# Optimization experiments

Hardware: AMD Instinct MI355X
Metric: run time of the kernel (lower is better)

## Reference

```python
import jax, jax.numpy as jnp
import numpy as np

B, T, C, H = 4, 2048, 1024, 16
D = C // H
SCALE = float(np.sqrt(C / H))  # quadf_scale = sqrt(D) = 8.0


def setup_inputs() -> dict:
    key = jax.random.key(0)
    k1, k2, k3 = jax.random.split(key, 3)
    x = jax.random.normal(k1, (B, T, C), dtype=jnp.float32)
    # torch Linear(C, 3C): y = x @ W.T; we store the transposed weight [C, 3C]
    W_attn = jax.random.normal(k2, (C, 3 * C), dtype=jnp.float32) * 0.02
    W_proj = jax.random.normal(k3, (C, C), dtype=jnp.float32) * 0.02
    return {"x": x, "W_attn": W_attn, "W_proj": W_proj}


def reference(x, W_attn, W_proj):
    # QKV projection
    qkv = x @ W_attn                      # [B, T, 3C]
    q, k, v = jnp.split(qkv, 3, axis=-1)  # each [B, T, C]

    def heads(t):  # [B, T, C] -> [B, H, T, D]
        return t.reshape(B, T, H, D).transpose(0, 2, 1, 3)

    q, k, v = heads(q), heads(k), heads(v)

    # scaled dot-product scores with causal mask
    scores = jnp.einsum("bhtd,bhsd->bhts", q, k) / SCALE  # [B, H, T, T]
    causal = jnp.tril(jnp.ones((T, T), dtype=bool))
    scores = jnp.where(causal, scores, -jnp.inf)
    attn = jax.nn.softmax(scores, axis=-1)
    # dropout = 0.0 (eval mode), so omitted

    y = jnp.einsum("bhts,bhsd->bhtd", attn, v)            # [B, H, T, D]
    y = y.transpose(0, 2, 1, 3).reshape(B, T, C)
    return y @ W_proj
```

## Files before the change

### kernel.cpp

```cpp
#include <hip/hip_runtime.h>
#include <hip/hip_bf16.h>

#define B_ 4
#define T_ 2048
#define C_ 1024
#define H_ 16
#define D_ 64
#define C3 3072

typedef __bf16 bf16x8 __attribute__((ext_vector_type(8)));
typedef __bf16 bf16x4 __attribute__((ext_vector_type(4)));
typedef float f32x2 __attribute__((ext_vector_type(2)));
typedef float f32x4 __attribute__((ext_vector_type(4)));
typedef float f32x16 __attribute__((ext_vector_type(16)));
typedef unsigned u32x4 __attribute__((ext_vector_type(4)));

#define SCALE_LOG2E 0.1803368801111244f

__device__ __forceinline__ void gload_lds16(const void* g, void* lds) {
  __builtin_amdgcn_global_load_lds((const __attribute__((address_space(1))) void*)g,
                                   (__attribute__((address_space(3))) void*)lds, 16, 0, 0);
}

__device__ __forceinline__ int swz128(int row, int chunk) {
  return row * 128 + ((chunk ^ (row & 7)) << 4);
}

__device__ __forceinline__ unsigned cvt_pk_bf16(float a, float b) {
  unsigned r;
  asm("v_cvt_pk_bf16_f32 %0, %1, %2" : "=v"(r) : "v"(a), "v"(b));
  return r;
}

__device__ __forceinline__ void pl32swap(unsigned& x, unsigned& y) {
  asm volatile("v_permlane32_swap_b32 %0, %1" : "+v"(x), "+v"(y));
}

__device__ __forceinline__ float fmax3(float a, float b, float c) {
  float d;
  asm("v_max3_f32 %0, %1, %2, %3" : "=v"(d) : "v"(a), "v"(b), "v"(c));
  return d;
}

__device__ __forceinline__ f32x2 pk_add(f32x2 a, f32x2 b) {
  f32x2 d;
  asm("v_pk_add_f32 %0, %1, %2" : "=v"(d) : "v"(a), "v"(b));
  return d;
}

__global__ void cast_x_kernel(const float* __restrict__ in, __bf16* __restrict__ out, int n4) {
  int i = blockIdx.x * blockDim.x + threadIdx.x;
  if (i >= n4) return;
  float4 v = ((const float4*)in)[i];
  bf16x4 o;
  o.x = (__bf16)v.x; o.y = (__bf16)v.y; o.z = (__bf16)v.z; o.w = (__bf16)v.w;
  ((bf16x4*)out)[i] = o;
}

__global__ void transpose_cast_kernel(const float* __restrict__ in, __bf16* __restrict__ out,
                                      int K, int N) {
  __shared__ float tile[32][33];
  int kb = blockIdx.y * 32, nb = blockIdx.x * 32;
  int tx = threadIdx.x, ty = threadIdx.y;
#pragma unroll
  for (int i = 0; i < 4; i++) {
    int r = ty + i * 8;
    tile[r][tx] = in[(size_t)(kb + r) * N + nb + tx];
  }
  __syncthreads();
#pragma unroll
  for (int i = 0; i < 4; i++) {
    int r = ty + i * 8;
    out[(size_t)(nb + r) * K + kb + tx] = (__bf16)tile[tx][r];
  }
}

template <int MODE>
__global__ __launch_bounds__(256) void gemm_bt_kernel(const __bf16* __restrict__ A,
                                                      const __bf16* __restrict__ Bt,
                                                      __bf16* __restrict__ Cb,
                                                      float* __restrict__ Cf,
                                                      __bf16* __restrict__ vT,
                                                      int M, int N, int K) {
  __shared__ char ldsbuf[2 * 128 * 128];
  char* ldsA = ldsbuf;
  char* ldsB = ldsbuf + 128 * 128;
  int tid = threadIdx.x, w = tid >> 6, l = tid & 63;
  int gx = gridDim.x;
  int nwg = gx * gridDim.y;
  int orig = blockIdx.y * gx + blockIdx.x;
  int cpx = nwg >> 3;
  int swz = (orig & 7) * cpx + (orig >> 3);
  int bx = swz % gx, by = swz / gx;
  int m0 = by * 128, n0 = bx * 128;
  int wr = w >> 1, wc = w & 1;
  int lr = l & 15, lhi = l >> 4;
  f32x4 acc[4][4];
#pragma unroll
  for (int m = 0; m < 4; m++)
#pragma unroll
    for (int n = 0; n < 4; n++) acc[m][n] = (f32x4){0.f, 0.f, 0.f, 0.f};

  int nK = K >> 6;
  for (int kt = 0; kt < nK; kt++) {
    int k0 = kt << 6;
    __syncthreads();
#pragma unroll
    for (int jj = 0; jj < 4; jj++) {
      int q = w * 4 + jj;
      int row = q * 8 + (l >> 3);
      int cg = (l & 7) ^ ((l >> 3) & 7);
      gload_lds16(A + (size_t)(m0 + row) * K + k0 + cg * 8, ldsA + q * 1024);
      gload_lds16(Bt + (size_t)(n0 + row) * K + k0 + cg * 8, ldsB + q * 1024);
    }
    __syncthreads();
    bf16x8 af[4][2], bfr[4][2];
#pragma unroll
    for (int m = 0; m < 4; m++) {
      int r = wr * 64 + m * 16 + lr;
#pragma unroll
      for (int kc = 0; kc < 2; kc++)
        af[m][kc] = *(const bf16x8*)(ldsA + swz128(r, kc * 4 + lhi));
    }
#pragma unroll
    for (int n = 0; n < 4; n++) {
      int r = wc * 64 + n * 16 + lr;
#pragma unroll
      for (int kc = 0; kc < 2; kc++)
        bfr[n][kc] = *(const bf16x8*)(ldsB + swz128(r, kc * 4 + lhi));
    }
#pragma unroll
    for (int kc = 0; kc < 2; kc++)
#pragma unroll
      for (int m = 0; m < 4; m++)
#pragma unroll
        for (int n = 0; n < 4; n++)
          acc[m][n] =
              __builtin_amdgcn_mfma_f32_16x16x32_bf16(af[m][kc], bfr[n][kc], acc[m][n], 0, 0, 0);
  }

  if (MODE == 2 && n0 >= 2048) {
    int bb = m0 >> 11;
    int tb = (m0 & 2047) + wr * 64 + lhi * 4;
#pragma unroll
    for (int n = 0; n < 4; n++) {
      int vcol = (n0 - 2048) + wc * 64 + n * 16 + lr;
      __bf16* vp = vT + ((size_t)bb * 1024 + vcol) * T_;
#pragma unroll
      for (int m = 0; m < 4; m++) {
        bf16x4 pv;
#pragma unroll
        for (int i = 0; i < 4; i++) pv[i] = (__bf16)acc[m][n][i];
        *(bf16x4*)(vp + tb + m * 16) = pv;
      }
    }
    return;
  }

  float oscale = (MODE == 2 && n0 < 1024) ? SCALE_LOG2E : 1.0f;
#pragma unroll
  for (int m = 0; m < 4; m++)
#pragma unroll
    for (int n = 0; n < 4; n++)
#pragma unroll
      for (int i = 0; i < 4; i++) {
        int rg = m0 + wr * 64 + m * 16 + lhi * 4 + i;
        int cg = n0 + wc * 64 + n * 16 + lr;
        if (MODE == 1)
          Cf[(size_t)rg * N + cg] = acc[m][n][i];
        else
          Cb[(size_t)rg * N + cg] = (__bf16)(acc[m][n][i] * oscale);
      }
}

__global__ __launch_bounds__(256) void attn_kernel(const __bf16* __restrict__ qkv,
                                                   const __bf16* __restrict__ vT,
                                                   __bf16* __restrict__ y) {
  __shared__ __align__(16) char lds[2][16384];
  int tid = threadIdx.x, w = tid >> 6, l = tid & 63;

  int g = blockIdx.x >> 6, bh = blockIdx.x & 63;
  int q2 = g >> 2;
  int qb = (q2 & 1) ? ((q2 == 1) ? g + 4 : g - 12) : (15 - g);
  int b = bh >> 4, h = bh & 15;
  size_t base = (size_t)b * T_ * C3;
  int lq = l & 31, hi = l >> 5;
  int qrow = qb * 128 + w * 32 + lq;
  int q0w = qb * 128 + w * 32;

  int lrow = l >> 3;
  int cg = (l & 7) ^ (lrow & 7);
  const __bf16* kptr = qkv + base + (size_t)(w * 16 + lrow) * C3 + C_ + h * D_ + cg * 8;
  const __bf16* vptr = vT + ((size_t)bh * D_ + w * 16 + lrow) * T_ + cg * 8;

  bf16x8 qf[4];
  {
    const __bf16* qp = qkv + base + (size_t)qrow * C3 + h * D_;
#pragma unroll
    for (int c = 0; c < 4; c++) qf[c] = *(const bf16x8*)(qp + c * 16 + hi * 8);
  }

  f32x16 zacc;
#pragma unroll
  for (int i = 0; i < 16; i++) zacc[i] = 0.f;
  f32x16 o[2];
  o[0] = zacc; o[1] = zacc;
  float mrun = -__builtin_inff(), lrun = 0.f;

  int nt = 2 * qb + 2;

  {
    char* kb = &lds[0][0];
    char* vb = &lds[0][8192];
    gload_lds16(kptr, kb + w * 2048);
    gload_lds16(kptr + 8 * C3, kb + w * 2048 + 1024);
    gload_lds16(vptr, vb + w * 2048);
    gload_lds16(vptr + 8 * T_, vb + w * 2048 + 1024);
  }

  for (int kt = 0; kt < nt; kt++) {
    int buf = kt & 1;
    __syncthreads();
    if (kt + 1 < nt) {
      char* kb = &lds[buf ^ 1][0];
      char* vb = &lds[buf ^ 1][8192];
      const __bf16* kp = kptr + (size_t)(kt + 1) * 64 * C3;
      const __bf16* vp = vptr + (kt + 1) * 64;
      gload_lds16(kp, kb + w * 2048);
      gload_lds16(kp + 8 * C3, kb + w * 2048 + 1024);
      gload_lds16(vp, vb + w * 2048);
      gload_lds16(vp + 8 * T_, vb + w * 2048 + 1024);
    }
    if (kt * 64 > q0w + 31) continue;
    char* kb = &lds[buf][0];
    char* vb = &lds[buf][8192];

    f32x16 s[2];
    __builtin_amdgcn_s_setprio(1);
#pragma unroll
    for (int b2 = 0; b2 < 2; b2++) {
      bf16x8 kf0 = *(const bf16x8*)(kb + swz128(b2 * 32 + lq, hi));
      s[b2] = __builtin_amdgcn_mfma_f32_32x32x16_bf16(kf0, qf[0], zacc, 0, 0, 0);
#pragma unroll
      for (int c = 1; c < 4; c++) {
        bf16x8 kf = *(const bf16x8*)(kb + swz128(b2 * 32 + lq, 2 * c + hi));
        s[b2] = __builtin_amdgcn_mfma_f32_32x32x16_bf16(kf, qf[c], s[b2], 0, 0, 0);
      }
    }
    __builtin_amdgcn_s_setprio(0);

    if (kt * 64 + 63 > q0w) {
#pragma unroll
      for (int b2 = 0; b2 < 2; b2++)
#pragma unroll
        for (int r = 0; r < 16; r++) {
          int kv = kt * 64 + b2 * 32 + ((r & 3) + 8 * (r >> 2)) + 4 * hi;
          if (kv > qrow) s[b2][r] = -1e30f;
        }
    }

    {
      auto xi = [&](int i) -> float { return i < 16 ? s[0][i] : s[1][i - 16]; };
      float t10[11];
#pragma unroll
      for (int g3 = 0; g3 < 10; g3++) t10[g3] = fmax3(xi(3 * g3), xi(3 * g3 + 1), xi(3 * g3 + 2));
      t10[10] = fmaxf(xi(30), xi(31));
      float u0 = fmax3(t10[0], t10[1], t10[2]);
      float u1 = fmax3(t10[3], t10[4], t10[5]);
      float u2 = fmax3(t10[6], t10[7], t10[8]);
      float u3 = fmaxf(t10[9], t10[10]);
      float tl = fmaxf(fmax3(u0, u1, u2), u3);
      float tmax = fmaxf(tl, __shfl_xor(tl, 32));

      if (!__all(tmax - mrun <= 8.0f)) {
        float mnew = fmaxf(mrun, tmax);
        float al = __builtin_amdgcn_exp2f(mrun - mnew);
        mrun = mnew;
        lrun *= al;
#pragma unroll
        for (int d = 0; d < 2; d++)
#pragma unroll
          for (int i = 0; i < 16; i++) o[d][i] *= al;
      }
    }

#pragma unroll
    for (int b2 = 0; b2 < 2; b2++)
#pragma unroll
      for (int r = 0; r < 16; r++) s[b2][r] = __builtin_amdgcn_exp2f(s[b2][r] - mrun);

    {
      f32x2 p8[8];
#pragma unroll
      for (int g3 = 0; g3 < 8; g3++) {
        f32x2 a = {s[0][2 * g3], s[0][2 * g3 + 1]};
        f32x2 b2v = {s[1][2 * g3], s[1][2 * g3 + 1]};
        p8[g3] = pk_add(a, b2v);
      }
#pragma unroll
      for (int g3 = 0; g3 < 4; g3++) p8[g3] = pk_add(p8[g3], p8[g3 + 4]);
      p8[0] = pk_add(p8[0], p8[2]);
      p8[1] = pk_add(p8[1], p8[3]);
      p8[0] = pk_add(p8[0], p8[1]);
      float rs = p8[0][0] + p8[0][1];
      lrun += rs + __shfl_xor(rs, 32);
    }

    bf16x8 pa[4];
#pragma unroll
    for (int b2 = 0; b2 < 2; b2++) {
      unsigned wg[4][2];
#pragma unroll
      for (int gg = 0; gg < 4; gg++) {
        wg[gg][0] = cvt_pk_bf16(s[b2][4 * gg + 0], s[b2][4 * gg + 1]);
        wg[gg][1] = cvt_pk_bf16(s[b2][4 * gg + 2], s[b2][4 * gg + 3]);
      }
#pragma unroll
      for (int cp = 0; cp < 2; cp++) {
        unsigned x0 = wg[2 * cp][0], x1 = wg[2 * cp][1];
        unsigned y0 = wg[2 * cp + 1][0], y1 = wg[2 * cp + 1][1];
        pl32swap(x0, y0);
        pl32swap(x1, y1);
        union { u32x4 u; bf16x8 hh; } uu;
        uu.u = (u32x4){x0, x1, y0, y1};
        pa[b2 * 2 + cp] = uu.hh;
      }
    }

    __builtin_amdgcn_s_setprio(1);
#pragma unroll
    for (int db = 0; db < 2; db++)
#pragma unroll
      for (int c = 0; c < 4; c++) {
        bf16x8 vf = *(const bf16x8*)(vb + swz128(db * 32 + lq, 2 * c + hi));
        o[db] = __builtin_amdgcn_mfma_f32_32x32x16_bf16(vf, pa[c], o[db], 0, 0, 0);
      }
    __builtin_amdgcn_s_setprio(0);
  }

  float inv = 1.f / lrun;
  __bf16* yp = y + (size_t)(b * T_ + qrow) * C_ + h * D_;
#pragma unroll
  for (int db = 0; db < 2; db++)
#pragma unroll
    for (int rr = 0; rr < 4; rr++) {
      bf16x4 ov;
#pragma unroll
      for (int i = 0; i < 4; i++) ov[i] = (__bf16)(o[db][rr * 4 + i] * inv);
      *(bf16x4*)(yp + db * 32 + rr * 8 + hi * 4) = ov;
    }
}

extern "C" void kernel_launch(void* const* d_in, const int* in_sizes, int n_in,
                              void* d_out, int out_size, void* d_ws, size_t ws_size,
                              hipStream_t stream) {
  const float* x = (const float*)d_in[0];
  const float* Wa = (const float*)d_in[1];
  const float* Wp = (const float*)d_in[2];
  float* out = (float*)d_out;
  char* ws = (char*)d_ws;

  __bf16* xb  = (__bf16*)(ws);
  __bf16* yb  = (__bf16*)(ws);
  __bf16* wat = (__bf16*)(ws + 16777216);
  __bf16* wpt = (__bf16*)(ws + 23068672);
  __bf16* qkv = (__bf16*)(ws + 25165824);
  __bf16* vT  = (__bf16*)(ws + 75497472);

  cast_x_kernel<<<8192, 256, 0, stream>>>(x, xb, (B_ * T_ * C_) / 4);
  transpose_cast_kernel<<<dim3(C3 / 32, C_ / 32), dim3(32, 8), 0, stream>>>(Wa, wat, C_, C3);
  transpose_cast_kernel<<<dim3(C_ / 32, C_ / 32), dim3(32, 8), 0, stream>>>(Wp, wpt, C_, C_);

  gemm_bt_kernel<2><<<dim3(C3 / 128, (B_ * T_) / 128), 256, 0, stream>>>(
      xb, wat, qkv, nullptr, vT, B_ * T_, C3, C_);

  attn_kernel<<<dim3(1024), 256, 0, stream>>>(qkv, vT, yb);

  gemm_bt_kernel<1><<<dim3(C_ / 128, (B_ * T_) / 128), 256, 0, stream>>>(
      yb, wpt, nullptr, out, nullptr, B_ * T_, C_, C_);
}
```

Measured before the change: 164.9 us.

## Rewrite GEMM as 256x256 tile, 8-wave double-buffered pipelined kernel

The bf16 GEMM moves from 128x128 tiles with 4 waves and a single LDS buffer to 256x256 tiles with 8 waves and 128KB of double-buffered LDS. Global-to-LDS loads for the next K-tile are issued in quarter-chunks inside each compute phase, gated by vmcnt waits and barriers, with setprio raised around the MFMA blocks. The goal is to overlap memory latency with MFMA work and raise per-tile data reuse. The cost is fewer workgroups (384 for QKV, 128 for the projection), which may underfill the CUs on the smaller GEMM, plus a fragile manual wait schedule.

Result: slower. 184.0 us (+11.5%).

```diff
diff --git a/kernel.cpp b/kernel.cpp
--- a/kernel.cpp
+++ b/kernel.cpp
@@ -76,78 +76,124 @@
 }
 
 template <int MODE>
-__global__ __launch_bounds__(256) void gemm_bt_kernel(const __bf16* __restrict__ A,
+__global__ __launch_bounds__(512) void gemm_bt_kernel(const __bf16* __restrict__ A,
                                                       const __bf16* __restrict__ Bt,
                                                       __bf16* __restrict__ Cb,
                                                       float* __restrict__ Cf,
                                                       __bf16* __restrict__ vT,
                                                       int M, int N, int K) {
-  __shared__ char ldsbuf[2 * 128 * 128];
-  char* ldsA = ldsbuf;
-  char* ldsB = ldsbuf + 128 * 128;
+  __shared__ __align__(16) char lds[131072];
   int tid = threadIdx.x, w = tid >> 6, l = tid & 63;
+  int wm = w >> 2, wn = w & 3;
+  int lr = l & 15, lhi = l >> 4;
+
   int gx = gridDim.x;
   int nwg = gx * gridDim.y;
   int orig = blockIdx.y * gx + blockIdx.x;
   int cpx = nwg >> 3;
   int swz = (orig & 7) * cpx + (orig >> 3);
   int bx = swz % gx, by = swz / gx;
-  int m0 = by * 128, n0 = bx * 128;
-  int wr = w >> 1, wc = w & 1;
-  int lr = l & 15, lhi = l >> 4;
-  f32x4 acc[4][4];
-#pragma unroll
-  for (int m = 0; m < 4; m++)
+  int m0 = by * 256, n0 = bx * 256;
+
+  const __bf16* Abase = A + (size_t)m0 * K;
+  const __bf16* Bbase = Bt + (size_t)n0 * K;
+
+  f32x4 acc[8][4];
+#pragma unroll
+  for (int m = 0; m < 8; m++)
 #pragma unroll
     for (int n = 0; n < 4; n++) acc[m][n] = (f32x4){0.f, 0.f, 0.f, 0.f};
 
-  int nK = K >> 6;
-  for (int kt = 0; kt < nK; kt++) {
+  int nKtot = K >> 6;
+  int lrow = l >> 3;
+  int cgs = (l & 7) ^ lrow;
+
+  auto stageu = [&](int u, int kt, int bufb) {
+    if (kt >= nKtot) kt = nKtot - 1;
     int k0 = kt << 6;
-    __syncthreads();
-#pragma unroll
-    for (int jj = 0; jj < 4; jj++) {
-      int q = w * 4 + jj;
-      int row = q * 8 + (l >> 3);
-      int cg = (l & 7) ^ ((l >> 3) & 7);
-      gload_lds16(A + (size_t)(m0 + row) * K + k0 + cg * 8, ldsA + q * 1024);
-      gload_lds16(Bt + (size_t)(n0 + row) * K + k0 + cg * 8, ldsB + q * 1024);
-    }
-    __syncthreads();
-    bf16x8 af[4][2], bfr[4][2];
-#pragma unroll
-    for (int m = 0; m < 4; m++) {
-      int r = wr * 64 + m * 16 + lr;
-#pragma unroll
-      for (int kc = 0; kc < 2; kc++)
-        af[m][kc] = *(const bf16x8*)(ldsA + swz128(r, kc * 4 + lhi));
-    }
-#pragma unroll
-    for (int n = 0; n < 4; n++) {
-      int r = wc * 64 + n * 16 + lr;
-#pragma unroll
-      for (int kc = 0; kc < 2; kc++)
-        bfr[n][kc] = *(const bf16x8*)(ldsB + swz128(r, kc * 4 + lhi));
-    }
-#pragma unroll
-    for (int kc = 0; kc < 2; kc++)
-#pragma unroll
-      for (int m = 0; m < 4; m++)
-#pragma unroll
-        for (int n = 0; n < 4; n++)
-          acc[m][n] =
-              __builtin_amdgcn_mfma_f32_16x16x32_bf16(af[m][kc], bfr[n][kc], acc[m][n], 0, 0, 0);
+    char* dA = lds + bufb * 65536;
+    char* dB = dA + 32768;
+#pragma unroll
+    for (int jj = 0; jj < 2; jj++) {
+      int j = w * 2 + jj;
+      if (u == 0 || u == 3) {
+        int q = (u == 3);
+        int rowbase = (j >> 3) * 128 + q * 64 + (j & 7) * 8;
+        gload_lds16(Abase + (size_t)(rowbase + lrow) * K + k0 + cgs * 8, dA + rowbase * 128);
+      } else {
+        int q = (u == 2);
+        int rowbase = (j >> 2) * 64 + q * 32 + (j & 3) * 8;
+        gload_lds16(Bbase + (size_t)(rowbase + lrow) * K + k0 + cgs * 8, dB + rowbase * 128);
+      }
+    }
+  };
+
+  stageu(0, 0, 0);
+  stageu(1, 0, 0);
+  stageu(2, 0, 0);
+  stageu(3, 0, 0);
+  asm volatile("s_waitcnt vmcnt(4)" ::: "memory");
+  __builtin_amdgcn_s_barrier();
+
+  int nIter = nKtot >> 1;
+  for (int it = 0; it < nIter; it++) {
+    int tS1 = 2 * it + 1;
+    int tS2 = 2 * it + 2;
+#pragma unroll
+    for (int ph = 0; ph < 8; ph++) {
+      const int grp = ph >> 2;
+      const int sub = ph & 3;
+      const int QM = sub >> 1, QN = sub & 1;
+      if (sub == 0)      asm volatile("s_waitcnt vmcnt(2)" ::: "memory");
+      else if (sub == 1) asm volatile("s_waitcnt vmcnt(4)" ::: "memory");
+      else if (sub == 2) asm volatile("s_waitcnt vmcnt(6)" ::: "memory");
+      else               asm volatile("s_waitcnt vmcnt(4)" ::: "memory");
+      char* lA = lds + grp * 65536;
+      char* lB = lA + 32768;
+      bf16x8 af[4][2], bfr[2][2];
+#pragma unroll
+      for (int mf = 0; mf < 4; mf++)
+#pragma unroll
+        for (int kk = 0; kk < 2; kk++)
+          af[mf][kk] =
+              *(const bf16x8*)(lA + swz128(wm * 128 + QM * 64 + mf * 16 + lr, kk * 4 + lhi));
+#pragma unroll
+      for (int nf = 0; nf < 2; nf++)
+#pragma unroll
+        for (int kk = 0; kk < 2; kk++)
+          bfr[nf][kk] =
+              *(const bf16x8*)(lB + swz128(wn * 64 + QN * 32 + nf * 16 + lr, kk * 4 + lhi));
+      {
+        int tS = grp == 0 ? tS1 : tS2;
+        int dstb = grp == 0 ? 1 : 0;
+        if (sub == 0) { stageu(0, tS, dstb); stageu(1, tS, dstb); }
+        else if (sub == 1) stageu(2, tS, dstb);
+        else if (sub == 2) stageu(3, tS, dstb);
+      }
+      __builtin_amdgcn_s_barrier();
+      __builtin_amdgcn_s_setprio(1);
+#pragma unroll
+      for (int kk = 0; kk < 2; kk++)
+#pragma unroll
+        for (int mf = 0; mf < 4; mf++)
+#pragma unroll
+          for (int nf = 0; nf < 2; nf++)
+            acc[QM * 4 + mf][QN * 2 + nf] = __builtin_amdgcn_mfma_f32_16x16x32_bf16(
+                af[mf][kk], bfr[nf][kk], acc[QM * 4 + mf][QN * 2 + nf], 0, 0, 0);
+      __builtin_amdgcn_s_setprio(0);
+      __builtin_amdgcn_s_barrier();
+    }
   }
 
   if (MODE == 2 && n0 >= 2048) {
     int bb = m0 >> 11;
-    int tb = (m0 & 2047) + wr * 64 + lhi * 4;
+    int tb = (m0 & 2047) + wm * 128 + lhi * 4;
 #pragma unroll
     for (int n = 0; n < 4; n++) {
-      int vcol = (n0 - 2048) + wc * 64 + n * 16 + lr;
+      int vcol = (n0 - 2048) + wn * 64 + n * 16 + lr;
       __bf16* vp = vT + ((size_t)bb * 1024 + vcol) * T_;
 #pragma unroll
-      for (int m = 0; m < 4; m++) {
+      for (int m = 0; m < 8; m++) {
         bf16x4 pv;
 #pragma unroll
         for (int i = 0; i < 4; i++) pv[i] = (__bf16)acc[m][n][i];
@@ -159,17 +205,17 @@
 
   float oscale = (MODE == 2 && n0 < 1024) ? SCALE_LOG2E : 1.0f;
 #pragma unroll
-  for (int m = 0; m < 4; m++)
+  for (int m = 0; m < 8; m++)
 #pragma unroll
     for (int n = 0; n < 4; n++)
 #pragma unroll
       for (int i = 0; i < 4; i++) {
-        int rg = m0 + wr * 64 + m * 16 + lhi * 4 + i;
-        int cg = n0 + wc * 64 + n * 16 + lr;
+        int rg = m0 + wm * 128 + m * 16 + lhi * 4 + i;
+        int cg2 = n0 + wn * 64 + n * 16 + lr;
         if (MODE == 1)
-          Cf[(size_t)rg * N + cg] = acc[m][n][i];
+          Cf[(size_t)rg * N + cg2] = acc[m][n][i];
         else
-          Cb[(size_t)rg * N + cg] = (__bf16)(acc[m][n][i] * oscale);
+          Cb[(size_t)rg * N + cg2] = (__bf16)(acc[m][n][i] * oscale);
       }
 }
 
@@ -371,11 +417,11 @@
   transpose_cast_kernel<<<dim3(C3 / 32, C_ / 32), dim3(32, 8), 0, stream>>>(Wa, wat, C_, C3);
   transpose_cast_kernel<<<dim3(C_ / 32, C_ / 32), dim3(32, 8), 0, stream>>>(Wp, wpt, C_, C_);
 
-  gemm_bt_kernel<2><<<dim3(C3 / 128, (B_ * T_) / 128), 256, 0, stream>>>(
+  gemm_bt_kernel<2><<<dim3(C3 / 256, (B_ * T_) / 256), 512, 0, stream>>>(
       xb, wat, qkv, nullptr, vT, B_ * T_, C3, C_);
 
   attn_kernel<<<dim3(1024), 256, 0, stream>>>(qkv, vT, yb);
 
-  gemm_bt_kernel<1><<<dim3(C_ / 128, (B_ * T_) / 128), 256, 0, stream>>>(
+  gemm_bt_kernel<1><<<dim3(C_ / 256, (B_ * T_) / 256), 512, 0, stream>>>(
       yb, wpt, nullptr, out, nullptr, B_ * T_, C_, C_);
 }
```
